# Kernel tuning notes

Measured on AMD Instinct MI355X. Metric: run time of the kernel, lower is better.

The kernel has to match this reference:

```python
import jax, jax.numpy as jnp
import numpy as np

D_MODEL = 1024
TEMPERATURE = 1.0

def setup_inputs() -> dict:
    key = jax.random.key(0)
    ks = jax.random.split(key, 9)
    B, NQ, NK, D = 4, 2048, 2048, D_MODEL
    s = 1.0 / np.sqrt(D)
    return {
        "Q": jax.random.normal(ks[0], (B, NQ, D), jnp.float32),
        "K": jax.random.normal(ks[1], (B, NK, D), jnp.float32),
        "V": jax.random.normal(ks[2], (B, NK, D), jnp.float32),
        "Wq": jax.random.normal(ks[3], (D, D), jnp.float32) * s,
        "bq": jax.random.normal(ks[4], (D,), jnp.float32) * 0.01,
        "Wk": jax.random.normal(ks[5], (D, D), jnp.float32) * s,
        "bk": jax.random.normal(ks[6], (D,), jnp.float32) * 0.01,
        "Wv": jax.random.normal(ks[7], (D, D), jnp.float32) * s,
        "bv": jax.random.normal(ks[8], (D,), jnp.float32) * 0.01,
    }

def reference(Q, K, V, Wq, bq, Wk, bk, Wv, bv):
    # torch nn.Linear: y = x @ W.T + b
    Qp = Q @ Wq.T + bq  # [B, NQ, D]
    Kp = K @ Wk.T + bk  # [B, NK, D]
    Vp = V @ Wv.T + bv  # [B, NK, D]

    # use_kl=True branch, vectorized:
    # kl[b,i,j] = D_KL(softmax(Kp[b,j]) || softmax(Qp[b,i]))
    #           = sum_d pK*(log pK - log pQ) = -H(pK_j) - pK_j . log pQ_i
    logpQ = jax.nn.log_softmax(Qp, axis=-1)  # [B, NQ, D]
    logpK = jax.nn.log_softmax(Kp, axis=-1)  # [B, NK, D]
    pK = jnp.exp(logpK)
    neg_ent_K = jnp.sum(pK * logpK, axis=-1)            # [B, NK], = -H(pK)
    cross = jnp.einsum('bjd,bid->bij', pK, logpQ)       # [B, NQ, NK]
    kl = neg_ent_K[:, None, :] - cross                  # [B, NQ, NK]
    scores = -kl / TEMPERATURE

    attn = jax.nn.softmax(scores, axis=-1)              # [B, NQ, NK]
    out = jnp.einsum('bij,bjd->bid', attn, Vp)          # [B, NQ, D]
    return out, attn
```

## Files before the change

kernel.cpp:

```cpp
#include <hip/hip_runtime.h>
#include <math.h>

#define D_MODEL 1024
#define NQS 2048
#define NKS 2048
#define BATCH 4

typedef __attribute__((ext_vector_type(8))) short bf16x8;
typedef __attribute__((ext_vector_type(4))) float f32x4;

#define AS1 __attribute__((address_space(1)))
#define AS3 __attribute__((address_space(3)))

__device__ __forceinline__ unsigned short f2bf(float f) {
  unsigned u = __builtin_bit_cast(unsigned, f);
  u = (u + 0x7FFF + ((u >> 16) & 1)) >> 16;
  return (unsigned short)u;
}
__device__ __forceinline__ float bf2f(unsigned short s) {
  return __builtin_bit_cast(float, ((unsigned)s) << 16);
}

__global__ __launch_bounds__(256) void cvt3_k(
    const float* __restrict__ s0, const float* __restrict__ s1,
    const float* __restrict__ s2, short* __restrict__ d0,
    short* __restrict__ d1, short* __restrict__ d2, int n8)
{
  const int z = blockIdx.z;
  const float* src = z == 0 ? s0 : (z == 1 ? s1 : s2);
  short* dst = z == 0 ? d0 : (z == 1 ? d1 : d2);
  int i = blockIdx.x * 256 + threadIdx.x;
  if (i >= n8) return;
  const float4 a = *(const float4*)&src[(long)i * 8];
  const float4 b = *(const float4*)&src[(long)i * 8 + 4];
  bf16x8 o;
  o[0] = (short)f2bf(a.x); o[1] = (short)f2bf(a.y);
  o[2] = (short)f2bf(a.z); o[3] = (short)f2bf(a.w);
  o[4] = (short)f2bf(b.x); o[5] = (short)f2bf(b.y);
  o[6] = (short)f2bf(b.z); o[7] = (short)f2bf(b.w);
  *(bf16x8*)&dst[(long)i * 8] = o;
}

__device__ __forceinline__ void gemm_tile_body(
    const short* __restrict__ Ab, const short* __restrict__ Bb,
    const float* __restrict__ bias, float bscale, float* __restrict__ Cf,
    short* __restrict__ Cbf, int N, int K, int gm, int gn)
{
  __shared__ short As[2][128 * 32];
  __shared__ short Bs[2][128 * 32];
  const int t = threadIdx.x;
  const int lane = t & 63, w = t >> 6;
  const int wm = w >> 1, wn = w & 1;

  const int srow = lane >> 2, sq = lane & 3;
  const short* gA0 = Ab + (long)(gm + w * 32 + srow) * K + sq * 8;
  const short* gA1 = Ab + (long)(gm + w * 32 + 16 + srow) * K + sq * 8;
  const short* gB0 = Bb + (long)(gn + w * 32 + srow) * K + sq * 8;
  const short* gB1 = Bb + (long)(gn + w * 32 + 16 + srow) * K + sq * 8;
  const int seg0 = (w * 2 + 0) * 512, seg1 = (w * 2 + 1) * 512;

  const int frow = lane & 15, fq = lane >> 4;

  f32x4 acc[4][4] = {};

  for (int k0 = 0; k0 < K; k0 += 64) {
#pragma unroll
    for (int p = 0; p < 2; ++p) {
      const int ko = k0 + p * 32;
      __builtin_amdgcn_global_load_lds((const AS1 void*)(gA0 + ko),
                                       (AS3 void*)(&As[p][seg0]), 16, 0, 0);
      __builtin_amdgcn_global_load_lds((const AS1 void*)(gA1 + ko),
                                       (AS3 void*)(&As[p][seg1]), 16, 0, 0);
      __builtin_amdgcn_global_load_lds((const AS1 void*)(gB0 + ko),
                                       (AS3 void*)(&Bs[p][seg0]), 16, 0, 0);
      __builtin_amdgcn_global_load_lds((const AS1 void*)(gB1 + ko),
                                       (AS3 void*)(&Bs[p][seg1]), 16, 0, 0);
    }
    __syncthreads();
#pragma unroll
    for (int p = 0; p < 2; ++p) {
      bf16x8 af[4], bfm[4];
#pragma unroll
      for (int mi = 0; mi < 4; ++mi)
        af[mi] =
            *(const bf16x8*)&As[p][(wm * 64 + mi * 16 + frow) * 32 + fq * 8];
#pragma unroll
      for (int ni = 0; ni < 4; ++ni)
        bfm[ni] =
            *(const bf16x8*)&Bs[p][(wn * 64 + ni * 16 + frow) * 32 + fq * 8];
#pragma unroll
      for (int mi = 0; mi < 4; ++mi)
#pragma unroll
        for (int ni = 0; ni < 4; ++ni)
          acc[mi][ni] = __builtin_amdgcn_mfma_f32_16x16x32_bf16(
              af[mi], bfm[ni], acc[mi][ni], 0, 0, 0);
    }
    __syncthreads();
  }

  float bb[4];
#pragma unroll
  for (int ni = 0; ni < 4; ++ni)
    bb[ni] = bias ? bias[gn + wn * 64 + ni * 16 + frow] * bscale : 0.f;

#pragma unroll
  for (int mi = 0; mi < 4; ++mi) {
#pragma unroll
    for (int r = 0; r < 4; ++r) {
      const long row = gm + wm * 64 + mi * 16 + fq * 4 + r;
#pragma unroll
      for (int ni = 0; ni < 4; ++ni) {
        const long col = gn + wn * 64 + ni * 16 + frow;
        float v = acc[mi][ni][r] + bb[ni];
        if (Cf) Cf[row * (long)N + col] = v;
        else    Cbf[row * (long)N + col] = (short)f2bf(v);
      }
    }
  }
}

__global__ __launch_bounds__(256, 4) void mfma_abt_k(
    const short* __restrict__ A, const short* __restrict__ B,
    const float* __restrict__ bias, float bscale, float* __restrict__ Cf,
    short* __restrict__ Cbf, int N, int K, long sA, long sB, long sC,
    long sBias, int swap)
{
  const int bz = blockIdx.z;
  const int gm = (swap ? blockIdx.x : blockIdx.y) * 128;
  const int gn = (swap ? blockIdx.y : blockIdx.x) * 128;
  gemm_tile_body(A + (long)bz * sA, B + (long)bz * sB,
                 bias ? bias + (long)bz * sBias : nullptr, bscale,
                 Cf ? Cf + (long)bz * sC : nullptr,
                 Cbf ? Cbf + (long)bz * sC : nullptr, N, K, gm, gn);
}

__global__ __launch_bounds__(256, 4) void mfma_proj_k(
    const short* __restrict__ Xq, const short* __restrict__ Xk,
    const short* __restrict__ Xv, const short* __restrict__ Wq,
    const short* __restrict__ Wk, const short* __restrict__ Wv,
    const float* __restrict__ bq, const float* __restrict__ bk,
    const float* __restrict__ bv, short* __restrict__ Oq,
    short* __restrict__ Ok, short* __restrict__ Ov)
{
  const int z = blockIdx.z;
  const short* X = z == 0 ? Xq : (z == 1 ? Xk : Xv);
  const short* W = z == 0 ? Wq : (z == 1 ? Wk : Wv);
  const float* bias = z == 0 ? bq : (z == 1 ? bk : bv);
  short* O = z == 0 ? Oq : (z == 1 ? Ok : Ov);
  gemm_tile_body(X, W, bias, 1.0f, nullptr, O, D_MODEL, D_MODEL,
                 blockIdx.x * 128, blockIdx.y * 128);
}

__global__ __launch_bounds__(256) void kstats_k(short* __restrict__ KP,
                                                float* __restrict__ negent)
{
  __shared__ float red[4];
  const long row = blockIdx.x;
  short* x = KP + row * (long)D_MODEL;
  const int t = threadIdx.x;
  short4 raw = *(const short4*)&x[t * 4];
  float v0 = bf2f((unsigned short)raw.x), v1 = bf2f((unsigned short)raw.y);
  float v2 = bf2f((unsigned short)raw.z), v3 = bf2f((unsigned short)raw.w);
  float m = fmaxf(fmaxf(v0, v1), fmaxf(v2, v3));
  for (int o = 32; o; o >>= 1) m = fmaxf(m, __shfl_xor(m, o));
  if ((t & 63) == 0) red[t >> 6] = m;
  __syncthreads();
  m = fmaxf(fmaxf(red[0], red[1]), fmaxf(red[2], red[3]));
  __syncthreads();
  float e0 = __expf(v0 - m), e1 = __expf(v1 - m), e2 = __expf(v2 - m),
        e3 = __expf(v3 - m);
  float s = e0 + e1 + e2 + e3;
  for (int o = 32; o; o >>= 1) s += __shfl_xor(s, o);
  if ((t & 63) == 0) red[t >> 6] = s;
  __syncthreads();
  s = red[0] + red[1] + red[2] + red[3];
  __syncthreads();
  const float inv = 1.0f / s;
  const float lse = m + __logf(s);
  float p0 = e0 * inv, p1 = e1 * inv, p2 = e2 * inv, p3 = e3 * inv;
  float ne = p0 * (v0 - lse) + p1 * (v1 - lse) + p2 * (v2 - lse) +
             p3 * (v3 - lse);
  for (int o = 32; o; o >>= 1) ne += __shfl_xor(ne, o);
  if ((t & 63) == 0) red[t >> 6] = ne;
  __syncthreads();
  if (t == 0) negent[row] = red[0] + red[1] + red[2] + red[3];
  short4 pw;
  pw.x = (short)f2bf(p0); pw.y = (short)f2bf(p1);
  pw.z = (short)f2bf(p2); pw.w = (short)f2bf(p3);
  *(short4*)&x[t * 4] = pw;
}

__global__ __launch_bounds__(256) void asoftmax_k(float* __restrict__ S,
                                                  short* __restrict__ Sbf)
{
  __shared__ float red[4];
  const long row = blockIdx.x;
  float* x = S + row * (long)NKS;
  short* y = Sbf + row * (long)NKS;
  const int t = threadIdx.x;
  float4 v0 = *(const float4*)&x[t * 4];
  float4 v1 = *(const float4*)&x[1024 + t * 4];
  float m = fmaxf(fmaxf(fmaxf(v0.x, v0.y), fmaxf(v0.z, v0.w)),
                  fmaxf(fmaxf(v1.x, v1.y), fmaxf(v1.z, v1.w)));
  for (int o = 32; o; o >>= 1) m = fmaxf(m, __shfl_xor(m, o));
  if ((t & 63) == 0) red[t >> 6] = m;
  __syncthreads();
  m = fmaxf(fmaxf(red[0], red[1]), fmaxf(red[2], red[3]));
  __syncthreads();
  float4 e0 = {__expf(v0.x - m), __expf(v0.y - m), __expf(v0.z - m),
               __expf(v0.w - m)};
  float4 e1 = {__expf(v1.x - m), __expf(v1.y - m), __expf(v1.z - m),
               __expf(v1.w - m)};
  float s = e0.x + e0.y + e0.z + e0.w + e1.x + e1.y + e1.z + e1.w;
  for (int o = 32; o; o >>= 1) s += __shfl_xor(s, o);
  if ((t & 63) == 0) red[t >> 6] = s;
  __syncthreads();
  s = red[0] + red[1] + red[2] + red[3];
  const float inv = 1.0f / s;
  float4 p0 = {e0.x * inv, e0.y * inv, e0.z * inv, e0.w * inv};
  float4 p1 = {e1.x * inv, e1.y * inv, e1.z * inv, e1.w * inv};
  *(float4*)&x[t * 4] = p0;
  *(float4*)&x[1024 + t * 4] = p1;
  short4 b0, b1;
  b0.x = (short)f2bf(p0.x); b0.y = (short)f2bf(p0.y);
  b0.z = (short)f2bf(p0.z); b0.w = (short)f2bf(p0.w);
  b1.x = (short)f2bf(p1.x); b1.y = (short)f2bf(p1.y);
  b1.z = (short)f2bf(p1.z); b1.w = (short)f2bf(p1.w);
  *(short4*)&y[t * 4] = b0;
  *(short4*)&y[1024 + t * 4] = b1;
}

__global__ __launch_bounds__(256) void transpose_k(const short* __restrict__ src,
                                                   short* __restrict__ dst)
{
  __shared__ short tile[64][68];
  const int j0 = blockIdx.x * 64;
  const int d0 = blockIdx.y * 64;
  const int t = threadIdx.x;
  const int r = t >> 2, c = t & 3;
#pragma unroll
  for (int i = 0; i < 4; ++i)
    *(short4*)&tile[r][c * 16 + i * 4] =
        *(const short4*)&src[(long)(j0 + r) * D_MODEL + d0 + c * 16 + i * 4];
  __syncthreads();
  const long b = j0 >> 11;
  const int jj = j0 & 2047;
#pragma unroll
  for (int i = 0; i < 4; ++i) {
    short4 o;
    o.x = tile[c * 16 + i * 4 + 0][r];
    o.y = tile[c * 16 + i * 4 + 1][r];
    o.z = tile[c * 16 + i * 4 + 2][r];
    o.w = tile[c * 16 + i * 4 + 3][r];
    *(short4*)&dst[b * ((long)D_MODEL * NKS) + (long)(d0 + r) * NKS + jj +
                   c * 16 + i * 4] = o;
  }
}

extern "C" void kernel_launch(void* const* d_in, const int* in_sizes, int n_in,
                              void* d_out, int out_size, void* d_ws,
                              size_t ws_size, hipStream_t stream)
{
  const float* Q = (const float*)d_in[0];
  const float* K = (const float*)d_in[1];
  const float* V = (const float*)d_in[2];
  const float* Wq = (const float*)d_in[3];
  const float* bq = (const float*)d_in[4];
  const float* Wk = (const float*)d_in[5];
  const float* bk = (const float*)d_in[6];
  const float* Wv = (const float*)d_in[7];
  const float* bv = (const float*)d_in[8];

  float* out = (float*)d_out;
  float* attn = out + (long)BATCH * NQS * D_MODEL;

  const long SZ = (long)BATCH * NQS * D_MODEL;
  short* ws = (short*)d_ws;
  short* Qbf = ws;
  short* Kbf = ws + SZ;
  short* Vbf = ws + 2 * SZ;
  short* Qp  = ws + 3 * SZ;
  short* pK  = ws + 4 * SZ;
  short* Vp  = ws + 5 * SZ;
  float* negent = (float*)(ws + 6 * SZ);
  short* attn_bf = ws;
  short* Vpt = ws + 2 * SZ;

  short* Wqb = (short*)attn;
  short* Wkb = Wqb + (long)D_MODEL * D_MODEL;
  short* Wvb = Wkb + (long)D_MODEL * D_MODEL;

  dim3 blk(256);
  const int n8x = (int)(SZ / 8);
  const int n8w = D_MODEL * D_MODEL / 8;

  cvt3_k<<<dim3(n8x / 256, 1, 3), blk, 0, stream>>>(Q, K, V, Qbf, Kbf, Vbf,
                                                    n8x);
  cvt3_k<<<dim3(n8w / 256, 1, 3), blk, 0, stream>>>(Wq, Wk, Wv, Wqb, Wkb, Wvb,
                                                    n8w);

  dim3 gp((BATCH * NQS) / 128, D_MODEL / 128, 3);
  mfma_proj_k<<<gp, blk, 0, stream>>>(Qbf, Kbf, Vbf, Wqb, Wkb, Wvb, bq, bk,
                                      bv, Qp, pK, Vp);

  kstats_k<<<dim3(BATCH * NKS), blk, 0, stream>>>(pK, negent);

  transpose_k<<<dim3((BATCH * NKS) / 64, D_MODEL / 64), blk, 0, stream>>>(Vp,
                                                                          Vpt);

  dim3 gs(NKS / 128, NQS / 128, BATCH);
  mfma_abt_k<<<gs, blk, 0, stream>>>(
      Qp, pK, negent, -1.0f, attn, nullptr, NKS, D_MODEL,
      (long)NQS * D_MODEL, (long)NKS * D_MODEL, (long)NQS * NKS, NKS, 0);

  asoftmax_k<<<dim3(BATCH * NQS), blk, 0, stream>>>(attn, attn_bf);

  dim3 go(NQS / 128, D_MODEL / 128, BATCH);
  mfma_abt_k<<<go, blk, 0, stream>>>(
      attn_bf, Vpt, nullptr, 0.f, out, nullptr, D_MODEL, NKS,
      (long)NQS * NKS, (long)D_MODEL * NKS, (long)NQS * D_MODEL, 0, 1);
}
```

Measured before the change: 377.2 us.

## Use 256x256 eight-wave GEMM with ping-pong LDS staging for projections and scores

Adds a 512-thread GEMM body that computes 256x256 output tiles. It double-buffers K-slices in LDS via direct global-to-LDS loads, interleaves staging of the next slice with MFMA phases, and uses setprio and barriers to schedule the waves. The body replaces the 128x128 kernel for the QKV projection and the score GEMM, which raises arithmetic intensity and cuts global traffic per FLOP. The final attn@V GEMM stays on the old kernel. Tradeoffs are fewer blocks, meaning less occupancy and tail balance, plus 64KB of LDS per block and more register pressure.

```diff
diff --git a/kernel.cpp b/kernel.cpp
--- a/kernel.cpp
+++ b/kernel.cpp
@@ -134,7 +134,199 @@
                  Cbf ? Cbf + (long)bz * sC : nullptr, N, K, gm, gn);
 }
 
-__global__ __launch_bounds__(256, 4) void mfma_proj_k(
+
+#define STAGE_HALF(gbase, hoff, kofs, region)                                \
+  do {                                                                       \
+    __builtin_amdgcn_global_load_lds(                                        \
+        (const AS1 void*)((gbase) + (long)(hoff) * K + (kofs)),              \
+        (AS3 void*)((region) + w * 512), 16, 0, 0);                          \
+    __builtin_amdgcn_global_load_lds(                                        \
+        (const AS1 void*)((gbase) + (long)((hoff) + 64) * K + (kofs)),       \
+        (AS3 void*)((region) + 4096 + w * 512), 16, 0, 0);                   \
+  } while (0)
+
+#define PHASE_TOP()                                  \
+  __builtin_amdgcn_s_barrier();                      \
+  asm volatile("s_waitcnt lgkmcnt(0)" ::: "memory"); \
+  __builtin_amdgcn_sched_barrier(0);                 \
+  __builtin_amdgcn_s_setprio(1)
+
+#define PHASE_END()                 \
+  __builtin_amdgcn_s_setprio(0);    \
+  __builtin_amdgcn_s_barrier();     \
+  __builtin_amdgcn_sched_barrier(0)
+
+template <int PI>
+__device__ __forceinline__ void tile4(short (&As)[2][2][8192],
+                                      short (&Bs)[2][2][8192],
+                                      const short* gA, const short* gB,
+                                      f32x4 (&acc)[8][4], int tau, int K,
+                                      int w, int wm, int wn, int frow,
+                                      int fq, int fr7)
+{
+  const int kt2 = (tau + 2) << 6;
+  const short* Ah = &As[PI][wm][0];
+  const short* Bh = &Bs[PI][wn >> 1][0];
+  const int bofs = (wn & 1) * 64;
+  const int x0 = (fq ^ fr7) * 8;
+  const int x1 = ((4 + fq) ^ fr7) * 8;
+
+  bf16x8 a0[4][2], a1[4][2], b0[2][2], b1[2][2];
+
+#pragma unroll
+  for (int mi = 0; mi < 4; ++mi) {
+    a0[mi][0] = *(const bf16x8*)&Ah[(mi * 16 + frow) * 64 + x0];
+    a0[mi][1] = *(const bf16x8*)&Ah[(mi * 16 + frow) * 64 + x1];
+  }
+#pragma unroll
+  for (int ni = 0; ni < 2; ++ni) {
+    b0[ni][0] = *(const bf16x8*)&Bh[(bofs + ni * 16 + frow) * 64 + x0];
+    b0[ni][1] = *(const bf16x8*)&Bh[(bofs + ni * 16 + frow) * 64 + x1];
+  }
+  PHASE_TOP();
+#pragma unroll
+  for (int kk = 0; kk < 2; ++kk)
+#pragma unroll
+    for (int mi = 0; mi < 4; ++mi)
+#pragma unroll
+      for (int ni = 0; ni < 2; ++ni)
+        acc[mi][ni] = __builtin_amdgcn_mfma_f32_16x16x32_bf16(
+            a0[mi][kk], b0[ni][kk], acc[mi][ni], 0, 0, 0);
+  PHASE_END();
+
+#pragma unroll
+  for (int ni = 0; ni < 2; ++ni) {
+    b1[ni][0] = *(const bf16x8*)&Bh[(bofs + 32 + ni * 16 + frow) * 64 + x0];
+    b1[ni][1] = *(const bf16x8*)&Bh[(bofs + 32 + ni * 16 + frow) * 64 + x1];
+  }
+  PHASE_TOP();
+#pragma unroll
+  for (int kk = 0; kk < 2; ++kk)
+#pragma unroll
+    for (int mi = 0; mi < 4; ++mi)
+#pragma unroll
+      for (int ni = 0; ni < 2; ++ni)
+        acc[mi][2 + ni] = __builtin_amdgcn_mfma_f32_16x16x32_bf16(
+            a0[mi][kk], b1[ni][kk], acc[mi][2 + ni], 0, 0, 0);
+  PHASE_END();
+
+#pragma unroll
+  for (int mi = 0; mi < 4; ++mi) {
+    a1[mi][0] = *(const bf16x8*)&Ah[(64 + mi * 16 + frow) * 64 + x0];
+    a1[mi][1] = *(const bf16x8*)&Ah[(64 + mi * 16 + frow) * 64 + x1];
+  }
+  if (kt2 < K) {
+    STAGE_HALF(gB, 0,   kt2, &Bs[PI][0][0]);
+    STAGE_HALF(gB, 128, kt2, &Bs[PI][1][0]);
+  }
+  PHASE_TOP();
+#pragma unroll
+  for (int kk = 0; kk < 2; ++kk)
+#pragma unroll
+    for (int mi = 0; mi < 4; ++mi)
+#pragma unroll
+      for (int ni = 0; ni < 2; ++ni)
+        acc[4 + mi][2 + ni] = __builtin_amdgcn_mfma_f32_16x16x32_bf16(
+            a1[mi][kk], b1[ni][kk], acc[4 + mi][2 + ni], 0, 0, 0);
+  PHASE_END();
+
+  if (kt2 < K) {
+    STAGE_HALF(gA, 0,   kt2, &As[PI][0][0]);
+    STAGE_HALF(gA, 128, kt2, &As[PI][1][0]);
+  }
+  __builtin_amdgcn_s_barrier();
+  __builtin_amdgcn_sched_barrier(0);
+  __builtin_amdgcn_s_setprio(1);
+#pragma unroll
+  for (int kk = 0; kk < 2; ++kk)
+#pragma unroll
+    for (int mi = 0; mi < 4; ++mi)
+#pragma unroll
+      for (int ni = 0; ni < 2; ++ni)
+        acc[4 + mi][ni] = __builtin_amdgcn_mfma_f32_16x16x32_bf16(
+            a1[mi][kk], b0[ni][kk], acc[4 + mi][ni], 0, 0, 0);
+  __builtin_amdgcn_s_setprio(0);
+  if (kt2 < K) asm volatile("s_waitcnt vmcnt(8)" ::: "memory");
+  else         asm volatile("s_waitcnt vmcnt(0)" ::: "memory");
+  __builtin_amdgcn_sched_barrier(0);
+  __builtin_amdgcn_s_barrier();
+  __builtin_amdgcn_sched_barrier(0);
+}
+
+__device__ __forceinline__ void gemm256_body(
+    const short* __restrict__ A, const short* __restrict__ B,
+    const float* __restrict__ bias, float bscale, float* __restrict__ Cf,
+    short* __restrict__ Cbf, int N, int K, int gm, int gn)
+{
+  __shared__ short As[2][2][8192];
+  __shared__ short Bs[2][2][8192];
+  const int t = threadIdx.x;
+  const int w = t >> 6, l = t & 63;
+  const int wm = w >> 2, wn = w & 3;
+  const int frow = l & 15, fq = l >> 4, fr7 = l & 7;
+  const int srow0 = w * 8 + (l >> 3);
+  const int sslot = (l & 7) ^ (l >> 3);
+
+  const short* gA = A + (long)(gm + srow0) * K + sslot * 8;
+  const short* gB = B + (long)(gn + srow0) * K + sslot * 8;
+
+  f32x4 acc[8][4] = {};
+
+  STAGE_HALF(gA, 0,   0,  &As[0][0][0]);
+  STAGE_HALF(gA, 128, 0,  &As[0][1][0]);
+  STAGE_HALF(gB, 0,   0,  &Bs[0][0][0]);
+  STAGE_HALF(gB, 128, 0,  &Bs[0][1][0]);
+  STAGE_HALF(gA, 0,   64, &As[1][0][0]);
+  STAGE_HALF(gA, 128, 64, &As[1][1][0]);
+  STAGE_HALF(gB, 0,   64, &Bs[1][0][0]);
+  STAGE_HALF(gB, 128, 64, &Bs[1][1][0]);
+  asm volatile("s_waitcnt vmcnt(8)" ::: "memory");
+  __builtin_amdgcn_s_barrier();
+  __builtin_amdgcn_sched_barrier(0);
+
+  const int NT = K >> 6;
+  for (int tau = 0; tau < NT; tau += 2) {
+    tile4<0>(As, Bs, gA, gB, acc, tau, K, w, wm, wn, frow, fq, fr7);
+    tile4<1>(As, Bs, gA, gB, acc, tau + 1, K, w, wm, wn, frow, fq, fr7);
+  }
+
+  float bb[4];
+#pragma unroll
+  for (int Ni = 0; Ni < 4; ++Ni)
+    bb[Ni] = bias ? bias[gn + wn * 64 + Ni * 16 + frow] * bscale : 0.f;
+
+#pragma unroll
+  for (int Mi = 0; Mi < 8; ++Mi) {
+#pragma unroll
+    for (int r = 0; r < 4; ++r) {
+      const long row = gm + wm * 128 + Mi * 16 + fq * 4 + r;
+#pragma unroll
+      for (int Ni = 0; Ni < 4; ++Ni) {
+        const long col = gn + wn * 64 + Ni * 16 + frow;
+        float v = acc[Mi][Ni][r] + bb[Ni];
+        if (Cf) Cf[row * (long)N + col] = v;
+        else    Cbf[row * (long)N + col] = (short)f2bf(v);
+      }
+    }
+  }
+}
+
+__global__ __launch_bounds__(512, 2) void mfma8_abt_k(
+    const short* __restrict__ A, const short* __restrict__ B,
+    const float* __restrict__ bias, float bscale, float* __restrict__ Cf,
+    short* __restrict__ Cbf, int N, int K, long sA, long sB, long sC,
+    long sBias, int swap)
+{
+  const int bz = blockIdx.z;
+  const int gm = (swap ? blockIdx.x : blockIdx.y) * 256;
+  const int gn = (swap ? blockIdx.y : blockIdx.x) * 256;
+  gemm256_body(A + (long)bz * sA, B + (long)bz * sB,
+               bias ? bias + (long)bz * sBias : nullptr, bscale,
+               Cf ? Cf + (long)bz * sC : nullptr,
+               Cbf ? Cbf + (long)bz * sC : nullptr, N, K, gm, gn);
+}
+
+__global__ __launch_bounds__(512, 2) void mfma8_proj_k(
     const short* __restrict__ Xq, const short* __restrict__ Xk,
     const short* __restrict__ Xv, const short* __restrict__ Wq,
     const short* __restrict__ Wk, const short* __restrict__ Wv,
@@ -147,8 +339,8 @@
   const short* W = z == 0 ? Wq : (z == 1 ? Wk : Wv);
   const float* bias = z == 0 ? bq : (z == 1 ? bk : bv);
   short* O = z == 0 ? Oq : (z == 1 ? Ok : Ov);
-  gemm_tile_body(X, W, bias, 1.0f, nullptr, O, D_MODEL, D_MODEL,
-                 blockIdx.x * 128, blockIdx.y * 128);
+  gemm256_body(X, W, bias, 1.0f, nullptr, O, D_MODEL, D_MODEL,
+               blockIdx.x * 256, blockIdx.y * 256);
 }
 
 __global__ __launch_bounds__(256) void kstats_k(short* __restrict__ KP,
@@ -290,7 +482,7 @@
   short* Wkb = Wqb + (long)D_MODEL * D_MODEL;
   short* Wvb = Wkb + (long)D_MODEL * D_MODEL;
 
-  dim3 blk(256);
+  dim3 blk(256), blk8(512);
   const int n8x = (int)(SZ / 8);
   const int n8w = D_MODEL * D_MODEL / 8;
 
@@ -299,17 +491,17 @@
   cvt3_k<<<dim3(n8w / 256, 1, 3), blk, 0, stream>>>(Wq, Wk, Wv, Wqb, Wkb, Wvb,
                                                     n8w);
 
-  dim3 gp((BATCH * NQS) / 128, D_MODEL / 128, 3);
-  mfma_proj_k<<<gp, blk, 0, stream>>>(Qbf, Kbf, Vbf, Wqb, Wkb, Wvb, bq, bk,
-                                      bv, Qp, pK, Vp);
+  dim3 gp((BATCH * NQS) / 256, D_MODEL / 256, 3);
+  mfma8_proj_k<<<gp, blk8, 0, stream>>>(Qbf, Kbf, Vbf, Wqb, Wkb, Wvb, bq, bk,
+                                        bv, Qp, pK, Vp);
 
   kstats_k<<<dim3(BATCH * NKS), blk, 0, stream>>>(pK, negent);
 
   transpose_k<<<dim3((BATCH * NKS) / 64, D_MODEL / 64), blk, 0, stream>>>(Vp,
                                                                           Vpt);
 
-  dim3 gs(NKS / 128, NQS / 128, BATCH);
-  mfma_abt_k<<<gs, blk, 0, stream>>>(
+  dim3 gs(NKS / 256, NQS / 256, BATCH);
+  mfma8_abt_k<<<gs, blk8, 0, stream>>>(
       Qp, pK, negent, -1.0f, attn, nullptr, NKS, D_MODEL,
       (long)NQS * D_MODEL, (long)NKS * D_MODEL, (long)NQS * NKS, NKS, 0);
 
```

After: 379.8 us. Within noise of the previous version (+0.7%).
